# Kernel tuning notes

Measured on AMD Instinct MI355X. Metric: run time of the kernel, lower is better.

Reference implementation:

```python
import jax, jax.numpy as jnp
import numpy as np
import math

N_HEAD = 16

def setup_inputs() -> dict:
    key = jax.random.key(0)
    k1, k2, k3 = jax.random.split(key, 3)
    B, S, D = 4, 2048, 1024
    hidden_states = jax.random.normal(k1, (B, S, D), dtype=jnp.float32)
    W_attn = jax.random.normal(k2, (D, 3 * D), dtype=jnp.float32) * 0.02
    b_attn = jnp.zeros((3 * D,), dtype=jnp.float32)
    W_proj = jax.random.normal(k3, (D, D), dtype=jnp.float32) * 0.02
    b_proj = jnp.zeros((D,), dtype=jnp.float32)
    return {"hidden_states": hidden_states, "W_attn": W_attn, "b_attn": b_attn,
            "W_proj": W_proj, "b_proj": b_proj}

def reference(hidden_states, W_attn, b_attn, W_proj, b_proj):
    B, S, D = hidden_states.shape
    H = N_HEAD
    hd = D // H
    # c_attn (GPT-2 Conv1D): x @ W + b -> [B, S, 3D]
    qkv = hidden_states @ W_attn + b_attn
    q, k, v = jnp.split(qkv, 3, axis=-1)
    # split heads -> [B, H, S, hd]
    def split_heads(t):
        return t.reshape(B, S, H, hd).transpose(0, 2, 1, 3)
    q, k, v = split_heads(q), split_heads(k), split_heads(v)
    # scores = QK^T / sqrt(hd)  -> [B, H, S, S]
    scores = jnp.einsum('bhqd,bhkd->bhqk', q, k) / math.sqrt(hd)
    # causal mask, multiplicative + additive as in source
    causal = jnp.tril(jnp.ones((S, S), dtype=scores.dtype))[None, None]
    scores = scores * causal + (-10000.0) * (1.0 - causal)
    attn_weights = jax.nn.softmax(scores, axis=-1)
    context = jnp.einsum('bhqk,bhkd->bhqd', attn_weights, v)
    # merge heads -> [B, S, D]
    attn_output = context.transpose(0, 2, 1, 3).reshape(B, S, D)
    # c_proj
    out = attn_output @ W_proj + b_proj
    return out
```

## Files before the change

kernel.cpp:

```cpp
#include <hip/hip_runtime.h>
#include <stdint.h>

typedef __attribute__((ext_vector_type(8))) short short8;
typedef __attribute__((ext_vector_type(8))) __bf16 bf16x8v;
typedef __attribute__((ext_vector_type(4))) float f32x4;

#define GLOBAL_AS __attribute__((address_space(1)))
#define LDS_AS __attribute__((address_space(3)))

__device__ __forceinline__ void gl2lds16(const void* g, void* l) {
  __builtin_amdgcn_global_load_lds((const GLOBAL_AS void*)g, (LDS_AS void*)l, 16, 0, 0);
}

__device__ __forceinline__ unsigned short f2bf(float x) {
  unsigned int u = __builtin_bit_cast(unsigned int, x);
  return (unsigned short)((u + 0x7fffu + ((u >> 16) & 1u)) >> 16);
}

__device__ __forceinline__ float bf2f(unsigned short u) {
  unsigned int v = (unsigned int)u << 16;
  return __builtin_bit_cast(float, v);
}

__device__ __forceinline__ unsigned cvtpk(float lo, float hi) {
  unsigned r;
  asm volatile("v_cvt_pk_bf16_f32 %0, %1, %2" : "=v"(r) : "v"(lo), "v"(hi));
  return r;
}

__device__ __forceinline__ short8 ldv8(const unsigned short* p) {
  return *(const short8*)p;
}

template <typename T>
__device__ __forceinline__ auto mfma_impl(T a, T b, f32x4 c, int)
    -> decltype(__builtin_amdgcn_mfma_f32_16x16x32_bf16(a, b, c, 0, 0, 0)) {
  return __builtin_amdgcn_mfma_f32_16x16x32_bf16(a, b, c, 0, 0, 0);
}
template <typename T>
__device__ __forceinline__ f32x4 mfma_impl(T a, T b, f32x4 c, long) {
  bf16x8v aa = __builtin_bit_cast(bf16x8v, a);
  bf16x8v bb = __builtin_bit_cast(bf16x8v, b);
  return __builtin_amdgcn_mfma_f32_16x16x32_bf16(aa, bb, c, 0, 0, 0);
}
__device__ __forceinline__ f32x4 mfma16(short8 a, short8 b, f32x4 c) {
  return mfma_impl(a, b, c, 0);
}

__global__ __launch_bounds__(256) void cast_bf16_kernel(const float* __restrict__ X,
                                                        unsigned short* __restrict__ Y,
                                                        int n4) {
  int i = blockIdx.x * 256 + threadIdx.x;
  if (i >= n4) return;
  const float4 v = ((const float4*)X)[i];
  unsigned long long pk = (unsigned long long)f2bf(v.x)
                        | ((unsigned long long)f2bf(v.y) << 16)
                        | ((unsigned long long)f2bf(v.z) << 32)
                        | ((unsigned long long)f2bf(v.w) << 48);
  ((unsigned long long*)Y)[i] = pk;
}

__global__ __launch_bounds__(256) void transpose_cast_kernel(const float* __restrict__ W,
                                                             unsigned short* __restrict__ Wt,
                                                             int Kd, int Nd) {
  __shared__ unsigned short tile[32][33];
  const int n0 = blockIdx.x * 32, k0 = blockIdx.y * 32;
  const int tx = threadIdx.x & 31, ty = threadIdx.x >> 5;
  #pragma unroll
  for (int i = 0; i < 4; ++i)
    tile[ty + i * 8][tx] = f2bf(W[(long)(k0 + ty + i * 8) * Nd + n0 + tx]);
  __syncthreads();
  #pragma unroll
  for (int i = 0; i < 4; ++i)
    Wt[(long)(n0 + ty + i * 8) * Kd + k0 + tx] = tile[tx][ty + i * 8];
}

template <int MODE>
__global__ __launch_bounds__(256) void gemm_kernel(
    const unsigned short* __restrict__ A,
    const unsigned short* __restrict__ Wt,
    const float* __restrict__ bias,
    float* __restrict__ Cout,
    unsigned short* __restrict__ Qb,
    unsigned short* __restrict__ Kb,
    unsigned short* __restrict__ Vt,
    int M, int N, int K) {
  __shared__ __align__(16) unsigned short Asm[128 * 32];
  __shared__ __align__(16) unsigned short Bsm[128 * 32];
  const int tid = threadIdx.x;
  const int w = tid >> 6, l = tid & 63;
  const int m0 = blockIdx.y * 128, n0 = blockIdx.x * 128;
  const int wr = (w >> 1) * 64, wc = (w & 1) * 64;
  const int laneRow = l & 15, laneG = l >> 4;

  const f32x4 z4 = {0.f, 0.f, 0.f, 0.f};
  f32x4 acc[4][4];
  #pragma unroll
  for (int m = 0; m < 4; ++m)
    #pragma unroll
    for (int n = 0; n < 4; ++n) acc[m][n] = z4;

  const int srow = tid >> 2;
  const int scol = (tid & 3) * 8;
  const unsigned short* Ag = A + (long)(m0 + srow) * K + scol;
  const unsigned short* Bg = Wt + (long)(n0 + srow) * K + scol;
  unsigned short* AsmW = Asm + w * 512;
  unsigned short* BsmW = Bsm + w * 512;

  const int aoff = (wr + laneRow) * 32 + laneG * 8;
  const int boff = (wc + laneRow) * 32 + laneG * 8;

  for (int kt = 0; kt < K; kt += 32) {
    gl2lds16(Ag + kt, AsmW);
    gl2lds16(Ag + (long)64 * K + kt, AsmW + 2048);
    gl2lds16(Bg + kt, BsmW);
    gl2lds16(Bg + (long)64 * K + kt, BsmW + 2048);
    __syncthreads();
    short8 af[4], bfr[4];
    #pragma unroll
    for (int m = 0; m < 4; ++m) af[m] = ldv8(Asm + aoff + m * 512);
    #pragma unroll
    for (int n = 0; n < 4; ++n) bfr[n] = ldv8(Bsm + boff + n * 512);
    #pragma unroll
    for (int m = 0; m < 4; ++m)
      #pragma unroll
      for (int n = 0; n < 4; ++n)
        acc[m][n] = mfma16(af[m], bfr[n], acc[m][n]);
    __syncthreads();
  }

  #pragma unroll
  for (int m = 0; m < 4; ++m) {
    const int row_base = m0 + wr + m * 16 + laneG * 4;
    #pragma unroll
    for (int n = 0; n < 4; ++n) {
      const int col = n0 + wc + n * 16 + laneRow;
      const float bv = bias[col];
      float v0 = acc[m][n][0] + bv;
      float v1 = acc[m][n][1] + bv;
      float v2 = acc[m][n][2] + bv;
      float v3 = acc[m][n][3] + bv;
      if (MODE == 1) {
        Cout[(long)(row_base + 0) * N + col] = v0;
        Cout[(long)(row_base + 1) * N + col] = v1;
        Cout[(long)(row_base + 2) * N + col] = v2;
        Cout[(long)(row_base + 3) * N + col] = v3;
      } else {
        const int which = col >> 10;
        const int d = col & 1023;
        const int h = d >> 6, e = d & 63;
        const int bb = row_base >> 11, s = row_base & 2047;
        if (which == 2) {
          unsigned long long pk = (unsigned long long)f2bf(v0)
                                | ((unsigned long long)f2bf(v1) << 16)
                                | ((unsigned long long)f2bf(v2) << 32)
                                | ((unsigned long long)f2bf(v3) << 48);
          *(unsigned long long*)(Vt + ((long)((bb * 16 + h) * 64 + e)) * 2048 + s) = pk;
        } else {
          unsigned short* T = (which == 0) ? Qb : Kb;
          long base = ((long)(bb * 16 + h) * 2048 + s) * 64 + e;
          T[base] = f2bf(v0);
          T[base + 64] = f2bf(v1);
          T[base + 128] = f2bf(v2);
          T[base + 192] = f2bf(v3);
        }
      }
    }
  }
}

__global__ __launch_bounds__(512) void attn_kernel(
    const unsigned short* __restrict__ Qb,
    const unsigned short* __restrict__ Kb,
    const unsigned short* __restrict__ Vt,
    unsigned short* __restrict__ Ao) {
  __shared__ __align__(16) unsigned short Ksm[2][64 * 64];
  __shared__ __align__(16) unsigned short Vsm[2][64 * 64];
  __shared__ __align__(16) unsigned short Psm[8][16][72];

  const int tid = threadIdx.x;
  const int w = tid >> 6, l = tid & 63;
  const int bid = blockIdx.x;
  const int px = bid >> 6;
  const int y = ((bid & 7) << 3) | ((bid >> 3) & 7);
  const int laneRow = l & 15, g = l >> 4;
  const unsigned short* Qh = Qb + (long)y * (2048 * 64);
  const unsigned short* Kh = Kb + (long)y * (2048 * 64);
  const unsigned short* Vh = Vt + (long)y * (64 * 2048);

  const int srow = tid >> 3;
  const int sxor = ((tid & 7) ^ (srow & 7)) * 8;
  const int b = y >> 4, h = y & 15;
  const f32x4 z4 = {0.f, 0.f, 0.f, 0.f};
  short8 ones8;
  #pragma unroll
  for (int j = 0; j < 8; ++j) ones8[j] = (short)0x3F80;

  auto STAGE = [&](int buf, int kt) {
    gl2lds16(Kh + (long)kt * 4096 + srow * 64 + sxor, &Ksm[buf][w * 512]);
    gl2lds16(Vh + kt * 64 + (long)srow * 2048 + sxor, &Vsm[buf][w * 512]);
  };

  for (int pass = 0; pass < 2; ++pass) {
    const int x = pass ? (15 - px) : px;
    const int q0 = x * 128;
    const int qlo = w * 16;

    const float QS = 0.18033688011112042f;
    short8 qf[2];
    {
      short8 r0 = ldv8(Qh + (q0 + qlo + laneRow) * 64 + g * 8);
      short8 r1 = ldv8(Qh + (q0 + qlo + laneRow) * 64 + 32 + g * 8);
      #pragma unroll
      for (int j = 0; j < 8; ++j) {
        qf[0][j] = (short)f2bf(bf2f((unsigned short)r0[j]) * QS);
        qf[1][j] = (short)f2bf(bf2f((unsigned short)r1[j]) * QS);
      }
    }

    float lr[4] = {0.f, 0.f, 0.f, 0.f};
    f32x4 o[4];
    #pragma unroll
    for (int i = 0; i < 4; ++i) o[i] = z4;

    const int nkt = 2 * x + 2;
    int cur = 0;
    STAGE(0, 0);
    asm volatile("s_waitcnt vmcnt(0)" ::: "memory");
    __builtin_amdgcn_s_barrier();

    for (int kt = 0; kt < nkt; ++kt) {
      if (kt + 1 < nkt) STAGE(cur ^ 1, kt + 1);

      const int keybase = kt * 64 - q0;
      const bool fullskip = keybase > qlo + 15;

      if (!fullskip) {
        f32x4 sc[4];
        __builtin_amdgcn_s_setprio(1);
        #pragma unroll
        for (int n = 0; n < 4; ++n) {
          const int krow = n * 16 + laneRow;
          short8 b0 = ldv8(&Ksm[cur][krow * 64 + ((g ^ (krow & 7)) * 8)]);
          short8 b1 = ldv8(&Ksm[cur][krow * 64 + (((g + 4) ^ (krow & 7)) * 8)]);
          f32x4 a = mfma16(b0, qf[0], z4);
          sc[n] = mfma16(b1, qf[1], a);
        }
        __builtin_amdgcn_s_setprio(0);

        if (keybase + 63 > qlo) {
          #pragma unroll
          for (int n = 0; n < 4; ++n) {
            const int keyb = keybase + n * 16 + g * 4;
            #pragma unroll
            for (int r = 0; r < 4; ++r)
              if (keyb + r > qlo + laneRow) sc[n][r] = -1e9f;
          }
        }

        #pragma unroll
        for (int n = 0; n < 4; ++n)
          #pragma unroll
          for (int r = 0; r < 4; ++r)
            sc[n][r] = exp2f(sc[n][r]);

        #pragma unroll
        for (int n = 0; n < 4; ++n) {
          uint2 pk;
          pk.x = cvtpk(sc[n][0], sc[n][1]);
          pk.y = cvtpk(sc[n][2], sc[n][3]);
          *(uint2*)&Psm[w][laneRow][n * 16 + g * 4] = pk;
        }
        asm volatile("s_waitcnt lgkmcnt(0)" ::: "memory");

        f32x4 rs = z4;
        #pragma unroll
        for (int kk = 0; kk < 2; ++kk) {
          short8 pf = ldv8(&Psm[w][laneRow][kk * 32 + g * 8]);
          __builtin_amdgcn_s_setprio(1);
          #pragma unroll
          for (int n2 = 0; n2 < 4; ++n2) {
            const int vrow = n2 * 16 + laneRow;
            short8 vf = ldv8(&Vsm[cur][vrow * 64 + (((g + kk * 4) ^ (vrow & 7)) * 8)]);
            o[n2] = mfma16(pf, vf, o[n2]);
          }
          rs = mfma16(pf, ones8, rs);
          __builtin_amdgcn_s_setprio(0);
        }
        #pragma unroll
        for (int r = 0; r < 4; ++r) lr[r] += rs[r];
      }

      asm volatile("s_waitcnt vmcnt(0)" ::: "memory");
      __builtin_amdgcn_s_barrier();
      cur ^= 1;
    }

    #pragma unroll
    for (int n2 = 0; n2 < 4; ++n2) {
      #pragma unroll
      for (int r = 0; r < 4; ++r) {
        float v = o[n2][r] / lr[r];
        long row = (long)b * 2048 + q0 + qlo + g * 4 + r;
        Ao[row * 1024 + h * 64 + n2 * 16 + laneRow] = f2bf(v);
      }
    }
  }
}

extern "C" void kernel_launch(void* const* d_in, const int* in_sizes, int n_in,
                              void* d_out, int out_size, void* d_ws, size_t ws_size,
                              hipStream_t stream) {
  const float* hs = (const float*)d_in[0];
  const float* W_attn = (const float*)d_in[1];
  const float* b_attn = (const float*)d_in[2];
  const float* W_proj = (const float*)d_in[3];
  const float* b_proj = (const float*)d_in[4];
  float* out = (float*)d_out;

  const size_t SZ_HS = 16777216;
  const size_t SZ_WA = 6291456;
  const size_t SZ_WP = 2097152;
  const size_t SZ_T = 16777216;
  if (ws_size < SZ_HS + SZ_WA + SZ_WP + 4 * SZ_T) return;

  char* p = (char*)d_ws;
  unsigned short* hs_bf = (unsigned short*)p; p += SZ_HS;
  unsigned short* WtA = (unsigned short*)p;   p += SZ_WA;
  unsigned short* WtP = (unsigned short*)p;   p += SZ_WP;
  unsigned short* Qb = (unsigned short*)p;    p += SZ_T;
  unsigned short* Kb = (unsigned short*)p;    p += SZ_T;
  unsigned short* Vt = (unsigned short*)p;    p += SZ_T;
  unsigned short* Ao = (unsigned short*)p;    p += SZ_T;

  cast_bf16_kernel<<<8192, 256, 0, stream>>>(hs, hs_bf, 8192 * 1024 / 4);
  transpose_cast_kernel<<<dim3(96, 32), 256, 0, stream>>>(W_attn, WtA, 1024, 3072);
  transpose_cast_kernel<<<dim3(32, 32), 256, 0, stream>>>(W_proj, WtP, 1024, 1024);
  gemm_kernel<0><<<dim3(24, 64), 256, 0, stream>>>(hs_bf, WtA, b_attn, nullptr, Qb, Kb, Vt,
                                                   8192, 3072, 1024);
  attn_kernel<<<512, 512, 0, stream>>>(Qb, Kb, Vt, Ao);
  gemm_kernel<1><<<dim3(8, 64), 256, 0, stream>>>(Ao, WtP, b_proj, out, nullptr, nullptr, nullptr,
                                                  8192, 1024, 1024);
}
```

Baseline: 190.8 us.

## Double-buffer GEMM LDS tiles and stage epilogue through LDS for vector stores

```diff
diff --git a/kernel.cpp b/kernel.cpp
--- a/kernel.cpp
+++ b/kernel.cpp
@@ -85,8 +85,8 @@
     unsigned short* __restrict__ Kb,
     unsigned short* __restrict__ Vt,
     int M, int N, int K) {
-  __shared__ __align__(16) unsigned short Asm[128 * 32];
-  __shared__ __align__(16) unsigned short Bsm[128 * 32];
+  __shared__ __align__(16) unsigned short Asm[2][128 * 32];
+  __shared__ __align__(16) unsigned short Bsm[2][128 * 32];
   const int tid = threadIdx.x;
   const int w = tid >> 6, l = tid & 63;
   const int m0 = blockIdx.y * 128, n0 = blockIdx.x * 128;
@@ -104,66 +104,98 @@
   const int scol = (tid & 3) * 8;
   const unsigned short* Ag = A + (long)(m0 + srow) * K + scol;
   const unsigned short* Bg = Wt + (long)(n0 + srow) * K + scol;
-  unsigned short* AsmW = Asm + w * 512;
-  unsigned short* BsmW = Bsm + w * 512;
 
   const int aoff = (wr + laneRow) * 32 + laneG * 8;
   const int boff = (wc + laneRow) * 32 + laneG * 8;
 
+  auto STAGE = [&](int buf, int kt) {
+    gl2lds16(Ag + kt, &Asm[buf][w * 512]);
+    gl2lds16(Ag + (long)64 * K + kt, &Asm[buf][2048 + w * 512]);
+    gl2lds16(Bg + kt, &Bsm[buf][w * 512]);
+    gl2lds16(Bg + (long)64 * K + kt, &Bsm[buf][2048 + w * 512]);
+  };
+
+  int cur = 0;
+  STAGE(0, 0);
+  asm volatile("s_waitcnt vmcnt(0)" ::: "memory");
+  __builtin_amdgcn_s_barrier();
+
   for (int kt = 0; kt < K; kt += 32) {
-    gl2lds16(Ag + kt, AsmW);
-    gl2lds16(Ag + (long)64 * K + kt, AsmW + 2048);
-    gl2lds16(Bg + kt, BsmW);
-    gl2lds16(Bg + (long)64 * K + kt, BsmW + 2048);
-    __syncthreads();
+    if (kt + 32 < K) STAGE(cur ^ 1, kt + 32);
     short8 af[4], bfr[4];
     #pragma unroll
-    for (int m = 0; m < 4; ++m) af[m] = ldv8(Asm + aoff + m * 512);
-    #pragma unroll
-    for (int n = 0; n < 4; ++n) bfr[n] = ldv8(Bsm + boff + n * 512);
+    for (int m = 0; m < 4; ++m) af[m] = ldv8(&Asm[cur][aoff + m * 512]);
+    #pragma unroll
+    for (int n = 0; n < 4; ++n) bfr[n] = ldv8(&Bsm[cur][boff + n * 512]);
     #pragma unroll
     for (int m = 0; m < 4; ++m)
       #pragma unroll
       for (int n = 0; n < 4; ++n)
         acc[m][n] = mfma16(af[m], bfr[n], acc[m][n]);
-    __syncthreads();
+    asm volatile("s_waitcnt vmcnt(0)" ::: "memory");
+    __builtin_amdgcn_s_barrier();
+    cur ^= 1;
   }
 
-  #pragma unroll
-  for (int m = 0; m < 4; ++m) {
-    const int row_base = m0 + wr + m * 16 + laneG * 4;
-    #pragma unroll
-    for (int n = 0; n < 4; ++n) {
-      const int col = n0 + wc + n * 16 + laneRow;
-      const float bv = bias[col];
-      float v0 = acc[m][n][0] + bv;
-      float v1 = acc[m][n][1] + bv;
-      float v2 = acc[m][n][2] + bv;
-      float v3 = acc[m][n][3] + bv;
-      if (MODE == 1) {
-        Cout[(long)(row_base + 0) * N + col] = v0;
-        Cout[(long)(row_base + 1) * N + col] = v1;
-        Cout[(long)(row_base + 2) * N + col] = v2;
-        Cout[(long)(row_base + 3) * N + col] = v3;
-      } else {
-        const int which = col >> 10;
+  if (MODE == 0 && n0 >= 2048) {
+    #pragma unroll
+    for (int m = 0; m < 4; ++m) {
+      const int row_base = m0 + wr + m * 16 + laneG * 4;
+      #pragma unroll
+      for (int n = 0; n < 4; ++n) {
+        const int col = n0 + wc + n * 16 + laneRow;
+        const float bv = bias[col];
         const int d = col & 1023;
         const int h = d >> 6, e = d & 63;
         const int bb = row_base >> 11, s = row_base & 2047;
-        if (which == 2) {
-          unsigned long long pk = (unsigned long long)f2bf(v0)
-                                | ((unsigned long long)f2bf(v1) << 16)
-                                | ((unsigned long long)f2bf(v2) << 32)
-                                | ((unsigned long long)f2bf(v3) << 48);
-          *(unsigned long long*)(Vt + ((long)((bb * 16 + h) * 64 + e)) * 2048 + s) = pk;
-        } else {
-          unsigned short* T = (which == 0) ? Qb : Kb;
-          long base = ((long)(bb * 16 + h) * 2048 + s) * 64 + e;
-          T[base] = f2bf(v0);
-          T[base + 64] = f2bf(v1);
-          T[base + 128] = f2bf(v2);
-          T[base + 192] = f2bf(v3);
-        }
+        unsigned long long pk = (unsigned long long)f2bf(acc[m][n][0] + bv)
+                              | ((unsigned long long)f2bf(acc[m][n][1] + bv) << 16)
+                              | ((unsigned long long)f2bf(acc[m][n][2] + bv) << 32)
+                              | ((unsigned long long)f2bf(acc[m][n][3] + bv) << 48);
+        *(unsigned long long*)(Vt + ((long)((bb * 16 + h) * 64 + e)) * 2048 + s) = pk;
+      }
+    }
+    return;
+  }
+
+  float* ep = ((w < 2) ? (float*)Asm : (float*)Bsm) + (w & 1) * 1088;
+  const int c0 = (l & 7) * 8;
+  const int rrow = l >> 3;
+  const int colg0 = n0 + wc + c0;
+  float bv[8];
+  #pragma unroll
+  for (int j = 0; j < 8; ++j) bv[j] = bias[colg0 + j];
+  unsigned short* Tqk = (colg0 >> 10) ? Kb : Qb;
+  const int hh = (colg0 & 1023) >> 6, e0 = colg0 & 63;
+
+  #pragma unroll
+  for (int m = 0; m < 4; ++m) {
+    asm volatile("s_waitcnt lgkmcnt(0)" ::: "memory");
+    #pragma unroll
+    for (int n = 0; n < 4; ++n)
+      #pragma unroll
+      for (int r = 0; r < 4; ++r)
+        ep[(laneG * 4 + r) * 68 + n * 16 + laneRow] = acc[m][n][r];
+    asm volatile("s_waitcnt lgkmcnt(0)" ::: "memory");
+    #pragma unroll
+    for (int j = 0; j < 2; ++j) {
+      const int row = rrow + j * 8;
+      f32x4 va = *(const f32x4*)&ep[row * 68 + c0];
+      f32x4 vb = *(const f32x4*)&ep[row * 68 + c0 + 4];
+      va[0] += bv[0]; va[1] += bv[1]; va[2] += bv[2]; va[3] += bv[3];
+      vb[0] += bv[4]; vb[1] += bv[5]; vb[2] += bv[6]; vb[3] += bv[7];
+      const int row_g = m0 + wr + m * 16 + row;
+      if (MODE == 1) {
+        *(f32x4*)&Cout[(long)row_g * N + colg0] = va;
+        *(f32x4*)&Cout[(long)row_g * N + colg0 + 4] = vb;
+      } else {
+        uint4 pk;
+        pk.x = cvtpk(va[0], va[1]);
+        pk.y = cvtpk(va[2], va[3]);
+        pk.z = cvtpk(vb[0], vb[1]);
+        pk.w = cvtpk(vb[2], vb[3]);
+        const int bb = row_g >> 11, s = row_g & 2047;
+        *(uint4*)(Tqk + ((long)(bb * 16 + hh) * 2048 + s) * 64 + e0) = pk;
       }
     }
   }
```

New measurement: 192.0 us. No clear change (+0.6%).
